# Optimization experiments

Hardware: AMD Instinct MI355X
Metric: run time of the kernel (lower is better)

The kernel has to match this reference:

```python
import jax, jax.numpy as jnp
import numpy as np

N_NODES = 100000
N_EDGES = 1600000
IN_SIZE = 128
HIDDEN = 32
OUT_SIZE = 16


def _mean_agg(h, src, dst, n_nodes):
    # segment-sum of source features into destination nodes, then divide by in-degree
    summed = jax.ops.segment_sum(h[src], dst, num_segments=n_nodes)  # [N, D]
    deg = jax.ops.segment_sum(jnp.ones((src.shape[0],), h.dtype), dst, num_segments=n_nodes)
    return summed / jnp.maximum(deg, 1.0)[:, None]


def _sage_layer(h, src, dst, W_self, W_neigh, b):
    # DGL SAGEConv (mean): fc_self(h) + fc_neigh(mean_neigh(h)) + bias
    agg = _mean_agg(h, src, dst, h.shape[0])
    return h @ W_self + agg @ W_neigh + b


def setup_inputs() -> dict:
    key = jax.random.key(0)
    ks = jax.random.split(key, 9)
    inp = {
        "x": jax.random.normal(ks[0], (N_NODES, IN_SIZE), jnp.float32),
        "edge_src": jax.random.randint(ks[1], (N_EDGES,), 0, N_NODES, jnp.int32),
        "edge_dst": jax.random.randint(ks[2], (N_EDGES,), 0, N_NODES, jnp.int32),
        "W_self1": jax.random.normal(ks[3], (IN_SIZE, HIDDEN), jnp.float32) / np.sqrt(IN_SIZE),
        "W_neigh1": jax.random.normal(ks[4], (IN_SIZE, HIDDEN), jnp.float32) / np.sqrt(IN_SIZE),
        "b1": jnp.zeros((HIDDEN,), jnp.float32),
        "W_self2": jax.random.normal(ks[5], (HIDDEN, HIDDEN), jnp.float32) / np.sqrt(HIDDEN),
        "W_neigh2": jax.random.normal(ks[6], (HIDDEN, HIDDEN), jnp.float32) / np.sqrt(HIDDEN),
        "b2": jnp.zeros((HIDDEN,), jnp.float32),
        "W_self3": jax.random.normal(ks[7], (HIDDEN, OUT_SIZE), jnp.float32) / np.sqrt(HIDDEN),
        "W_neigh3": jax.random.normal(ks[8], (HIDDEN, OUT_SIZE), jnp.float32) / np.sqrt(HIDDEN),
        "b3": jnp.zeros((OUT_SIZE,), jnp.float32),
    }
    return inp


def reference(x, edge_src, edge_dst,
              W_self1, W_neigh1, b1,
              W_self2, W_neigh2, b2,
              W_self3, W_neigh3, b3):
    h = jax.nn.relu(_sage_layer(x, edge_src, edge_dst, W_self1, W_neigh1, b1))
    h = jax.nn.relu(_sage_layer(h, edge_src, edge_dst, W_self2, W_neigh2, b2))
    h = _sage_layer(h, edge_src, edge_dst, W_self3, W_neigh3, b3)
    return h
```

## Files before the change

### kernel.cpp

```cpp
#include <hip/hip_runtime.h>


#define BLOCK 256
#define NBLK 256
#define BSH 9
#define CAP 12288

__device__ __forceinline__ unsigned pack_bf16(float a, float b) {
    unsigned ua = __float_as_uint(a); ua = (ua + 0x7fffu + ((ua >> 16) & 1u)) >> 16;
    unsigned ub = __float_as_uint(b); ub = (ub + 0x7fffu + ((ub >> 16) & 1u)) >> 16;
    return ua | (ub << 16);
}

__global__ void hist_kernel(const int* __restrict__ dst, int* __restrict__ hist,
                            int n_edges, int nbuk, int ch) {
    __shared__ int cnt[256];
    int tid = threadIdx.x;
    for (int i = tid; i < nbuk; i += BLOCK) cnt[i] = 0;
    __syncthreads();
    int e0 = blockIdx.x * ch;
    int e1 = e0 + ch; if (e1 > n_edges) e1 = n_edges;
    for (int e = e0 + tid; e < e1; e += BLOCK)
        atomicAdd(&cnt[dst[e] >> BSH], 1);
    __syncthreads();
    for (int i = tid; i < nbuk; i += BLOCK)
        hist[i * NBLK + blockIdx.x] = cnt[i];
}

__global__ void scanBlk_kernel(int* __restrict__ hist, int* __restrict__ buktot) {
    int b = blockIdx.x;
    int tid = threadIdx.x;
    int orig = hist[b * NBLK + tid];
    int v = orig;
    int lane = tid & 63, w = tid >> 6;
#pragma unroll
    for (int off = 1; off < 64; off <<= 1) {
        int u = __shfl_up(v, off);
        if (lane >= off) v += u;
    }
    __shared__ int wps[4];
    if (lane == 63) wps[w] = v;
    __syncthreads();
    int wadd = 0;
    for (int k = 0; k < w; ++k) wadd += wps[k];
    int excl = v - orig + wadd;
    hist[b * NBLK + tid] = excl;
    if (tid == 255) buktot[b] = excl + orig;
}

__global__ void scanBuk_kernel(const int* __restrict__ buktot, int* __restrict__ bukoff,
                               int nbuk, int* __restrict__ startp, int n_nodes, int n_edges) {
    int tid = threadIdx.x;
    int orig = (tid < nbuk) ? buktot[tid] : 0;
    int v = orig;
    int lane = tid & 63, w = tid >> 6;
#pragma unroll
    for (int off = 1; off < 64; off <<= 1) {
        int u = __shfl_up(v, off);
        if (lane >= off) v += u;
    }
    __shared__ int wps[4];
    if (lane == 63) wps[w] = v;
    __syncthreads();
    int wadd = 0;
    for (int k = 0; k < w; ++k) wadd += wps[k];
    int excl = v - orig + wadd;
    if (tid < nbuk) bukoff[tid] = excl;
    if (tid == 0) { bukoff[nbuk] = n_edges; startp[n_nodes] = n_edges; }
}

__global__ void part_kernel(const int* __restrict__ src, const int* __restrict__ dst,
                            const int* __restrict__ hist, const int* __restrict__ bukoff,
                            unsigned* __restrict__ pairs, int n_edges, int nbuk, int ch) {
    __shared__ int base[256];
    __shared__ int cnt[256];
    int tid = threadIdx.x;
    for (int i = tid; i < nbuk; i += BLOCK) {
        base[i] = hist[i * NBLK + blockIdx.x] + bukoff[i];
        cnt[i] = 0;
    }
    __syncthreads();
    int e0 = blockIdx.x * ch;
    int e1 = e0 + ch; if (e1 > n_edges) e1 = n_edges;
    for (int e = e0 + tid; e < e1; e += BLOCK) {
        int d = dst[e];
        int b = d >> BSH;
        unsigned dl = (unsigned)(d & ((1 << BSH) - 1));
        int r = atomicAdd(&cnt[b], 1);
        pairs[base[b] + r] = (unsigned)src[e] | (dl << 20);
    }
}

__global__ void build_kernel(const unsigned* __restrict__ pairs, const int* __restrict__ bukoff,
                             int* __restrict__ start, float* __restrict__ invdeg,
                             int* __restrict__ csr_src, int n_nodes) {
    __shared__ int deg[512];
    __shared__ int lst[512];
    __shared__ int cur[512];
    __shared__ int wps[4];
    __shared__ int scsr[CAP];

    int b = blockIdx.x;
    int tid = threadIdx.x;
    int e0 = bukoff[b];
    int e1 = bukoff[b + 1];
    int lo = b << BSH;
    int hi = lo + (1 << BSH); if (hi > n_nodes) hi = n_nodes;
    int nn = hi - lo;
    int ne = e1 - e0;

    for (int i = tid; i < 512; i += BLOCK) deg[i] = 0;
    __syncthreads();
    for (int i = e0 + tid; i < e1; i += BLOCK)
        atomicAdd(&deg[pairs[i] >> 20], 1);
    __syncthreads();

    int d0 = deg[2 * tid], d1 = deg[2 * tid + 1];
    int s = d0 + d1;
    int lane = tid & 63, w = tid >> 6;
    int v = s;
#pragma unroll
    for (int off = 1; off < 64; off <<= 1) {
        int u = __shfl_up(v, off);
        if (lane >= off) v += u;
    }
    if (lane == 63) wps[w] = v;
    __syncthreads();
    int wb = 0;
    for (int k = 0; k < w; ++k) wb += wps[k];
    int excl = wb + v - s;
    lst[2 * tid] = excl;
    lst[2 * tid + 1] = excl + d0;
    cur[2 * tid] = 0;
    cur[2 * tid + 1] = 0;
    __syncthreads();

    for (int i = tid; i < nn; i += BLOCK) {
        start[lo + i] = e0 + lst[i];
        int d = deg[i];
        invdeg[lo + i] = 1.0f / (float)(d < 1 ? 1 : d);
    }

    if (ne <= CAP) {
        for (int i = e0 + tid; i < e1; i += BLOCK) {
            unsigned pr = pairs[i];
            int dl = pr >> 20;
            int sl = lst[dl] + atomicAdd(&cur[dl], 1);
            scsr[sl] = (int)(pr & 0xFFFFFu);
        }
        __syncthreads();
        for (int i = tid; i < ne; i += BLOCK) csr_src[e0 + i] = scsr[i];
    } else {
        for (int i = e0 + tid; i < e1; i += BLOCK) {
            unsigned pr = pairs[i];
            int dl = pr >> 20;
            int sl = lst[dl] + atomicAdd(&cur[dl], 1);
            csr_src[e0 + sl] = (int)(pr & 0xFFFFFu);
        }
    }
}

template<int DIN, int DOUT, int OPT, int NPT>
__global__ __launch_bounds__(256, 4)
void proj_reg(const float* __restrict__ h,
              const float* __restrict__ Ws,
              const float* __restrict__ Wn,
              const float* __restrict__ bias,
              float* __restrict__ pre,
              unsigned short* __restrict__ p,
              int n_nodes) {
    constexpr int OD  = 2 * DOUT;
    constexpr int OG  = OD / OPT;
    constexpr int NG  = 256 / OG;
    constexpr int NT  = NPT * NG;
    constexpr int NV  = OPT / 4;

    __shared__ float sW[DIN][OD];
    __shared__ float sb[DOUT];

    const int tid = threadIdx.x;
    for (int i = tid; i < DIN * OD; i += 256) {
        int k = i / OD, o = i % OD;
        sW[k][o] = (o < DOUT) ? Ws[k * DOUT + o] : Wn[k * DOUT + (o - DOUT)];
    }
    if (tid < DOUT) sb[tid] = bias[tid];
    __syncthreads();

    const int to = tid % OG;
    const int tn = tid / OG;
    const int o0 = to * OPT;
    const int node0 = blockIdx.x * NT + tn * NPT;

    const float4* __restrict__ xp[NPT];
#pragma unroll
    for (int n = 0; n < NPT; ++n) {
        int node = node0 + n;
        int safe = (node < n_nodes) ? node : (n_nodes - 1);
        xp[n] = reinterpret_cast<const float4*>(h + (size_t)safe * DIN);
    }

    float acc[NPT][OPT];
#pragma unroll
    for (int n = 0; n < NPT; ++n)
#pragma unroll
        for (int o = 0; o < OPT; ++o) acc[n][o] = 0.f;

#pragma unroll 2
    for (int k4 = 0; k4 < DIN / 4; ++k4) {
        float4 xv[NPT];
#pragma unroll
        for (int n = 0; n < NPT; ++n) xv[n] = xp[n][k4];
#pragma unroll
        for (int kk = 0; kk < 4; kk += 2) {
            int k = 4 * k4 + kk;
            float4 w0[NV], w1[NV];
#pragma unroll
            for (int v = 0; v < NV; ++v) {
                w0[v] = *reinterpret_cast<const float4*>(&sW[k][o0 + 4 * v]);
                w1[v] = *reinterpret_cast<const float4*>(&sW[k + 1][o0 + 4 * v]);
            }
#pragma unroll
            for (int n = 0; n < NPT; ++n) {
                float xk = reinterpret_cast<const float*>(&xv[n])[kk];
#pragma unroll
                for (int v = 0; v < NV; ++v) {
                    acc[n][4 * v + 0] = fmaf(xk, w0[v].x, acc[n][4 * v + 0]);
                    acc[n][4 * v + 1] = fmaf(xk, w0[v].y, acc[n][4 * v + 1]);
                    acc[n][4 * v + 2] = fmaf(xk, w0[v].z, acc[n][4 * v + 2]);
                    acc[n][4 * v + 3] = fmaf(xk, w0[v].w, acc[n][4 * v + 3]);
                }
            }
#pragma unroll
            for (int n = 0; n < NPT; ++n) {
                float xk = reinterpret_cast<const float*>(&xv[n])[kk + 1];
#pragma unroll
                for (int v = 0; v < NV; ++v) {
                    acc[n][4 * v + 0] = fmaf(xk, w1[v].x, acc[n][4 * v + 0]);
                    acc[n][4 * v + 1] = fmaf(xk, w1[v].y, acc[n][4 * v + 1]);
                    acc[n][4 * v + 2] = fmaf(xk, w1[v].z, acc[n][4 * v + 2]);
                    acc[n][4 * v + 3] = fmaf(xk, w1[v].w, acc[n][4 * v + 3]);
                }
            }
        }
    }

    const bool self_half = (o0 < DOUT);
    const int oo = self_half ? o0 : (o0 - DOUT);
#pragma unroll
    for (int n = 0; n < NPT; ++n) {
        int node = node0 + n;
        if (node >= n_nodes) continue;
        if (self_half) {
#pragma unroll
            for (int v = 0; v < NV; ++v) {
                float4 r;
                r.x = acc[n][4 * v + 0] + sb[oo + 4 * v + 0];
                r.y = acc[n][4 * v + 1] + sb[oo + 4 * v + 1];
                r.z = acc[n][4 * v + 2] + sb[oo + 4 * v + 2];
                r.w = acc[n][4 * v + 3] + sb[oo + 4 * v + 3];
                *reinterpret_cast<float4*>(pre + (size_t)node * DOUT + oo + 4 * v) = r;
            }
        } else {
            unsigned uw[OPT / 2];
#pragma unroll
            for (int v = 0; v < OPT / 2; ++v)
                uw[v] = pack_bf16(acc[n][2 * v], acc[n][2 * v + 1]);
            unsigned short* dstp = p + (size_t)node * DOUT + oo;
            if (OPT == 8) {
                *reinterpret_cast<uint4*>(dstp) = make_uint4(uw[0], uw[1], uw[2], uw[3]);
            } else {
                *reinterpret_cast<uint2*>(dstp) = make_uint2(uw[0], uw[1]);
            }
        }
    }
}

template<int D, bool RELU>
__global__ void gather_kernel(const unsigned short* __restrict__ p,
                              const int* __restrict__ csr_src,
                              const int* __restrict__ start,
                              const float* __restrict__ pre,
                              const float* __restrict__ invdeg,
                              float* __restrict__ out,
                              int n_nodes) {
    constexpr int NPW = 64 / D;
    int wave = threadIdx.x >> 6;
    int lane = threadIdx.x & 63;
    int g = (blockIdx.x * (blockDim.x >> 6) + wave) * NPW + lane / D;
    int f = lane % D;
    if (g >= n_nodes) return;
    int s0 = start[g];
    int s1 = start[g + 1];
    float a0 = 0.f, a1 = 0.f, a2 = 0.f, a3 = 0.f;
    float a4 = 0.f, a5 = 0.f, a6 = 0.f, a7 = 0.f;
    int j = s0;
    for (; j + 8 <= s1; j += 8) {
        int c0 = csr_src[j + 0], c1 = csr_src[j + 1];
        int c2 = csr_src[j + 2], c3 = csr_src[j + 3];
        int c4 = csr_src[j + 4], c5 = csr_src[j + 5];
        int c6 = csr_src[j + 6], c7 = csr_src[j + 7];
        unsigned short u0 = p[(size_t)c0 * D + f];
        unsigned short u1 = p[(size_t)c1 * D + f];
        unsigned short u2 = p[(size_t)c2 * D + f];
        unsigned short u3 = p[(size_t)c3 * D + f];
        unsigned short u4 = p[(size_t)c4 * D + f];
        unsigned short u5 = p[(size_t)c5 * D + f];
        unsigned short u6 = p[(size_t)c6 * D + f];
        unsigned short u7 = p[(size_t)c7 * D + f];
        a0 += __uint_as_float((unsigned)u0 << 16);
        a1 += __uint_as_float((unsigned)u1 << 16);
        a2 += __uint_as_float((unsigned)u2 << 16);
        a3 += __uint_as_float((unsigned)u3 << 16);
        a4 += __uint_as_float((unsigned)u4 << 16);
        a5 += __uint_as_float((unsigned)u5 << 16);
        a6 += __uint_as_float((unsigned)u6 << 16);
        a7 += __uint_as_float((unsigned)u7 << 16);
    }
    for (; j + 2 <= s1; j += 2) {
        int c0 = csr_src[j], c1 = csr_src[j + 1];
        a0 += __uint_as_float((unsigned)p[(size_t)c0 * D + f] << 16);
        a1 += __uint_as_float((unsigned)p[(size_t)c1 * D + f] << 16);
    }
    if (j < s1)
        a2 += __uint_as_float((unsigned)p[(size_t)csr_src[j] * D + f] << 16);
    float a = ((a0 + a1) + (a2 + a3)) + ((a4 + a5) + (a6 + a7));
    size_t o = (size_t)g * D + f;
    float v = pre[o] + a * invdeg[g];
    if (RELU) v = fmaxf(v, 0.f);
    out[o] = v;
}

extern "C" void kernel_launch(void* const* d_in, const int* in_sizes, int n_in,
                              void* d_out, int out_size, void* d_ws, size_t ws_size,
                              hipStream_t stream) {
    const float* x        = (const float*)d_in[0];
    const int*   edge_src = (const int*)d_in[1];
    const int*   edge_dst = (const int*)d_in[2];
    const float* Ws1 = (const float*)d_in[3];
    const float* Wn1 = (const float*)d_in[4];
    const float* b1  = (const float*)d_in[5];
    const float* Ws2 = (const float*)d_in[6];
    const float* Wn2 = (const float*)d_in[7];
    const float* b2  = (const float*)d_in[8];
    const float* Ws3 = (const float*)d_in[9];
    const float* Wn3 = (const float*)d_in[10];
    const float* b3  = (const float*)d_in[11];
    float* out = (float*)d_out;

    const int IN = 128, HID = 32;
    const int n_nodes = in_sizes[0] / IN;
    const int n_edges = in_sizes[1];
    const int nbuk = (n_nodes + (1 << BSH) - 1) >> BSH;
    const int ch   = (n_edges + NBLK - 1) / NBLK;

    char* wsb = (char*)d_ws;
    size_t off = 0;
    auto alloc = [&](size_t bytes) { char* r = wsb + off; off = (off + bytes + 255) & ~(size_t)255; return r; };
    int*   startp = (int*)alloc(((size_t)n_nodes + 1) * sizeof(int));
    float* invdeg = (float*)alloc((size_t)n_nodes * sizeof(float));
    int*   csr    = (int*)alloc((size_t)n_edges * sizeof(int));
    int*   hist   = (int*)alloc((size_t)nbuk * NBLK * sizeof(int));
    int*   buktot = (int*)alloc(256 * sizeof(int));
    int*   bukoff = (int*)alloc(257 * sizeof(int));
    float* B0     = (float*)alloc((size_t)n_nodes * HID * sizeof(float));
    unsigned short* B1 = (unsigned short*)alloc((size_t)n_nodes * HID * 2);
    float* B3     = (float*)alloc((size_t)n_nodes * HID * sizeof(float));
    unsigned* pairs = (unsigned*)B0;

    const int gP     = (n_nodes + 63) / 64;
    const int gGat32 = (n_nodes + 7) / 8;
    const int gGat16 = (n_nodes + 15) / 16;

    hist_kernel   <<<NBLK, BLOCK, 0, stream>>>(edge_dst, hist, n_edges, nbuk, ch);
    scanBlk_kernel<<<nbuk, BLOCK, 0, stream>>>(hist, buktot);
    scanBuk_kernel<<<1, BLOCK, 0, stream>>>(buktot, bukoff, nbuk, startp, n_nodes, n_edges);
    part_kernel   <<<NBLK, BLOCK, 0, stream>>>(edge_src, edge_dst, hist, bukoff, pairs, n_edges, nbuk, ch);
    build_kernel  <<<nbuk, BLOCK, 0, stream>>>(pairs, bukoff, startp, invdeg, csr, n_nodes);

    proj_reg<128, 32, 8, 2><<<gP, BLOCK, 0, stream>>>(x, Ws1, Wn1, b1, B0, B1, n_nodes);
    gather_kernel<32, true><<<gGat32, BLOCK, 0, stream>>>(B1, csr, startp, B0, invdeg, B3, n_nodes);

    proj_reg<32, 32, 8, 2><<<gP, BLOCK, 0, stream>>>(B3, Ws2, Wn2, b2, B0, B1, n_nodes);
    gather_kernel<32, true><<<gGat32, BLOCK, 0, stream>>>(B1, csr, startp, B0, invdeg, B3, n_nodes);

    proj_reg<32, 16, 4, 2><<<gP, BLOCK, 0, stream>>>(B3, Ws3, Wn3, b3, B0, B1, n_nodes);
    gather_kernel<16, false><<<gGat16, BLOCK, 0, stream>>>(B1, csr, startp, B0, invdeg, out, n_nodes);
}
```

Baseline: 196.3 us.

## Use bf16 MFMA for node projections and store hidden activations as bf16

```diff
diff --git a/kernel.cpp b/kernel.cpp
--- a/kernel.cpp
+++ b/kernel.cpp
@@ -6,10 +6,17 @@
 #define BSH 9
 #define CAP 12288
 
+typedef __attribute__((ext_vector_type(8))) short bf16x8;
+typedef __attribute__((ext_vector_type(4))) float f32x4;
+
 __device__ __forceinline__ unsigned pack_bf16(float a, float b) {
     unsigned ua = __float_as_uint(a); ua = (ua + 0x7fffu + ((ua >> 16) & 1u)) >> 16;
     unsigned ub = __float_as_uint(b); ub = (ub + 0x7fffu + ((ub >> 16) & 1u)) >> 16;
     return ua | (ub << 16);
+}
+__device__ __forceinline__ unsigned short bf16r(float f) {
+    unsigned u = __float_as_uint(f);
+    return (unsigned short)((u + 0x7fffu + ((u >> 16) & 1u)) >> 16);
 }
 
 __global__ void hist_kernel(const int* __restrict__ dst, int* __restrict__ hist,
@@ -160,128 +167,138 @@
     }
 }
 
-template<int DIN, int DOUT, int OPT, int NPT>
+__global__ void prep_kernel(const float* __restrict__ Ws1, const float* __restrict__ Wn1,
+                            const float* __restrict__ Ws2, const float* __restrict__ Wn2,
+                            const float* __restrict__ Ws3, const float* __restrict__ Wn3,
+                            unsigned short* __restrict__ Wt1,
+                            unsigned short* __restrict__ Wt2,
+                            unsigned short* __restrict__ Wt3) {
+    int stride = gridDim.x * BLOCK;
+    int t0 = blockIdx.x * BLOCK + threadIdx.x;
+    for (int i = t0; i < 64 * 128; i += stride) {
+        int o = i / 128, k = i % 128;
+        float v = (o < 32) ? Ws1[k * 32 + o] : Wn1[k * 32 + (o - 32)];
+        Wt1[i] = bf16r(v);
+    }
+    for (int i = t0; i < 64 * 32; i += stride) {
+        int o = i / 32, k = i % 32;
+        float v = (o < 32) ? Ws2[k * 32 + o] : Wn2[k * 32 + (o - 32)];
+        Wt2[i] = bf16r(v);
+    }
+    for (int i = t0; i < 32 * 32; i += stride) {
+        int o = i / 32, k = i % 32;
+        float v = (o < 16) ? Ws3[k * 16 + o] : Wn3[k * 16 + (o - 16)];
+        Wt3[i] = bf16r(v);
+    }
+}
+
 __global__ __launch_bounds__(256, 4)
-void proj_reg(const float* __restrict__ h,
-              const float* __restrict__ Ws,
-              const float* __restrict__ Wn,
-              const float* __restrict__ bias,
-              float* __restrict__ pre,
-              unsigned short* __restrict__ p,
-              int n_nodes) {
-    constexpr int OD  = 2 * DOUT;
-    constexpr int OG  = OD / OPT;
-    constexpr int NG  = 256 / OG;
-    constexpr int NT  = NPT * NG;
-    constexpr int NV  = OPT / 4;
-
-    __shared__ float sW[DIN][OD];
-    __shared__ float sb[DOUT];
-
-    const int tid = threadIdx.x;
-    for (int i = tid; i < DIN * OD; i += 256) {
-        int k = i / OD, o = i % OD;
-        sW[k][o] = (o < DOUT) ? Ws[k * DOUT + o] : Wn[k * DOUT + (o - DOUT)];
-    }
-    if (tid < DOUT) sb[tid] = bias[tid];
-    __syncthreads();
-
-    const int to = tid % OG;
-    const int tn = tid / OG;
-    const int o0 = to * OPT;
-    const int node0 = blockIdx.x * NT + tn * NPT;
-
-    const float4* __restrict__ xp[NPT];
-#pragma unroll
-    for (int n = 0; n < NPT; ++n) {
-        int node = node0 + n;
-        int safe = (node < n_nodes) ? node : (n_nodes - 1);
-        xp[n] = reinterpret_cast<const float4*>(h + (size_t)safe * DIN);
-    }
-
-    float acc[NPT][OPT];
-#pragma unroll
-    for (int n = 0; n < NPT; ++n)
-#pragma unroll
-        for (int o = 0; o < OPT; ++o) acc[n][o] = 0.f;
-
-#pragma unroll 2
-    for (int k4 = 0; k4 < DIN / 4; ++k4) {
-        float4 xv[NPT];
-#pragma unroll
-        for (int n = 0; n < NPT; ++n) xv[n] = xp[n][k4];
-#pragma unroll
-        for (int kk = 0; kk < 4; kk += 2) {
-            int k = 4 * k4 + kk;
-            float4 w0[NV], w1[NV];
-#pragma unroll
-            for (int v = 0; v < NV; ++v) {
-                w0[v] = *reinterpret_cast<const float4*>(&sW[k][o0 + 4 * v]);
-                w1[v] = *reinterpret_cast<const float4*>(&sW[k + 1][o0 + 4 * v]);
-            }
-#pragma unroll
-            for (int n = 0; n < NPT; ++n) {
-                float xk = reinterpret_cast<const float*>(&xv[n])[kk];
-#pragma unroll
-                for (int v = 0; v < NV; ++v) {
-                    acc[n][4 * v + 0] = fmaf(xk, w0[v].x, acc[n][4 * v + 0]);
-                    acc[n][4 * v + 1] = fmaf(xk, w0[v].y, acc[n][4 * v + 1]);
-                    acc[n][4 * v + 2] = fmaf(xk, w0[v].z, acc[n][4 * v + 2]);
-                    acc[n][4 * v + 3] = fmaf(xk, w0[v].w, acc[n][4 * v + 3]);
-                }
-            }
-#pragma unroll
-            for (int n = 0; n < NPT; ++n) {
-                float xk = reinterpret_cast<const float*>(&xv[n])[kk + 1];
-#pragma unroll
-                for (int v = 0; v < NV; ++v) {
-                    acc[n][4 * v + 0] = fmaf(xk, w1[v].x, acc[n][4 * v + 0]);
-                    acc[n][4 * v + 1] = fmaf(xk, w1[v].y, acc[n][4 * v + 1]);
-                    acc[n][4 * v + 2] = fmaf(xk, w1[v].z, acc[n][4 * v + 2]);
-                    acc[n][4 * v + 3] = fmaf(xk, w1[v].w, acc[n][4 * v + 3]);
-                }
+void proj1_mfma(const float* __restrict__ x,
+                const unsigned short* __restrict__ Wt,
+                const float* __restrict__ bias,
+                float* __restrict__ pre,
+                unsigned short* __restrict__ p,
+                int n_nodes) {
+    int tid = threadIdx.x;
+    int wv = tid >> 6, l = tid & 63;
+    int col = l & 15, kg = l >> 4;
+    int node0 = blockIdx.x * 64 + wv * 16;
+
+    int arow = node0 + col;
+    if (arow >= n_nodes) arow = n_nodes - 1;
+    const float* xr = x + (size_t)arow * 128 + kg * 8;
+
+    f32x4 acc[4];
+#pragma unroll
+    for (int t = 0; t < 4; ++t) acc[t] = (f32x4){0.f, 0.f, 0.f, 0.f};
+
+#pragma unroll
+    for (int ks = 0; ks < 4; ++ks) {
+        float4 f0 = *reinterpret_cast<const float4*>(xr + ks * 32);
+        float4 f1 = *reinterpret_cast<const float4*>(xr + ks * 32 + 4);
+        union { bf16x8 v; unsigned u[4]; } A;
+        A.u[0] = pack_bf16(f0.x, f0.y);
+        A.u[1] = pack_bf16(f0.z, f0.w);
+        A.u[2] = pack_bf16(f1.x, f1.y);
+        A.u[3] = pack_bf16(f1.z, f1.w);
+#pragma unroll
+        for (int t = 0; t < 4; ++t) {
+            bf16x8 B = *reinterpret_cast<const bf16x8*>(
+                Wt + (size_t)(t * 16 + col) * 128 + ks * 32 + kg * 8);
+            acc[t] = __builtin_amdgcn_mfma_f32_16x16x32_bf16(A.v, B, acc[t], 0, 0, 0);
+        }
+    }
+
+    int nodeb = node0 + kg * 4;
+#pragma unroll
+    for (int t = 0; t < 4; ++t) {
+        int out = t * 16 + col;
+#pragma unroll
+        for (int r = 0; r < 4; ++r) {
+            int node = nodeb + r;
+            if (node >= n_nodes) continue;
+            if (t < 2) {
+                pre[(size_t)node * 32 + out] = acc[t][r] + bias[out];
+            } else {
+                p[(size_t)node * 32 + (out - 32)] = bf16r(acc[t][r]);
             }
         }
     }
-
-    const bool self_half = (o0 < DOUT);
-    const int oo = self_half ? o0 : (o0 - DOUT);
-#pragma unroll
-    for (int n = 0; n < NPT; ++n) {
-        int node = node0 + n;
-        if (node >= n_nodes) continue;
-        if (self_half) {
-#pragma unroll
-            for (int v = 0; v < NV; ++v) {
-                float4 r;
-                r.x = acc[n][4 * v + 0] + sb[oo + 4 * v + 0];
-                r.y = acc[n][4 * v + 1] + sb[oo + 4 * v + 1];
-                r.z = acc[n][4 * v + 2] + sb[oo + 4 * v + 2];
-                r.w = acc[n][4 * v + 3] + sb[oo + 4 * v + 3];
-                *reinterpret_cast<float4*>(pre + (size_t)node * DOUT + oo + 4 * v) = r;
-            }
-        } else {
-            unsigned uw[OPT / 2];
-#pragma unroll
-            for (int v = 0; v < OPT / 2; ++v)
-                uw[v] = pack_bf16(acc[n][2 * v], acc[n][2 * v + 1]);
-            unsigned short* dstp = p + (size_t)node * DOUT + oo;
-            if (OPT == 8) {
-                *reinterpret_cast<uint4*>(dstp) = make_uint4(uw[0], uw[1], uw[2], uw[3]);
+}
+
+template<int DOUT>
+__global__ __launch_bounds__(256, 4)
+void proj23_mfma(const unsigned short* __restrict__ h,
+                 const unsigned short* __restrict__ Wt,
+                 const float* __restrict__ bias,
+                 float* __restrict__ pre,
+                 unsigned short* __restrict__ p,
+                 int n_nodes) {
+    constexpr int NTILE = DOUT / 8;
+    int tid = threadIdx.x;
+    int wv = tid >> 6, l = tid & 63;
+    int col = l & 15, kg = l >> 4;
+    int node0 = blockIdx.x * 64 + wv * 16;
+
+    int arow = node0 + col;
+    if (arow >= n_nodes) arow = n_nodes - 1;
+    bf16x8 A = *reinterpret_cast<const bf16x8*>(h + (size_t)arow * 32 + kg * 8);
+
+    f32x4 acc[NTILE];
+#pragma unroll
+    for (int t = 0; t < NTILE; ++t) acc[t] = (f32x4){0.f, 0.f, 0.f, 0.f};
+
+#pragma unroll
+    for (int t = 0; t < NTILE; ++t) {
+        bf16x8 B = *reinterpret_cast<const bf16x8*>(
+            Wt + (size_t)(t * 16 + col) * 32 + kg * 8);
+        acc[t] = __builtin_amdgcn_mfma_f32_16x16x32_bf16(A, B, acc[t], 0, 0, 0);
+    }
+
+    int nodeb = node0 + kg * 4;
+#pragma unroll
+    for (int t = 0; t < NTILE; ++t) {
+        int out = t * 16 + col;
+#pragma unroll
+        for (int r = 0; r < 4; ++r) {
+            int node = nodeb + r;
+            if (node >= n_nodes) continue;
+            if (out < DOUT) {
+                pre[(size_t)node * DOUT + out] = acc[t][r] + bias[out];
             } else {
-                *reinterpret_cast<uint2*>(dstp) = make_uint2(uw[0], uw[1]);
+                p[(size_t)node * DOUT + (out - DOUT)] = bf16r(acc[t][r]);
             }
         }
     }
 }
 
-template<int D, bool RELU>
+template<int D, bool RELU, bool BF16OUT>
 __global__ void gather_kernel(const unsigned short* __restrict__ p,
                               const int* __restrict__ csr_src,
                               const int* __restrict__ start,
                               const float* __restrict__ pre,
                               const float* __restrict__ invdeg,
-                              float* __restrict__ out,
+                              void* __restrict__ outv,
                               int n_nodes) {
     constexpr int NPW = 64 / D;
     int wave = threadIdx.x >> 6;
@@ -299,22 +316,14 @@
         int c2 = csr_src[j + 2], c3 = csr_src[j + 3];
         int c4 = csr_src[j + 4], c5 = csr_src[j + 5];
         int c6 = csr_src[j + 6], c7 = csr_src[j + 7];
-        unsigned short u0 = p[(size_t)c0 * D + f];
-        unsigned short u1 = p[(size_t)c1 * D + f];
-        unsigned short u2 = p[(size_t)c2 * D + f];
-        unsigned short u3 = p[(size_t)c3 * D + f];
-        unsigned short u4 = p[(size_t)c4 * D + f];
-        unsigned short u5 = p[(size_t)c5 * D + f];
-        unsigned short u6 = p[(size_t)c6 * D + f];
-        unsigned short u7 = p[(size_t)c7 * D + f];
-        a0 += __uint_as_float((unsigned)u0 << 16);
-        a1 += __uint_as_float((unsigned)u1 << 16);
-        a2 += __uint_as_float((unsigned)u2 << 16);
-        a3 += __uint_as_float((unsigned)u3 << 16);
-        a4 += __uint_as_float((unsigned)u4 << 16);
-        a5 += __uint_as_float((unsigned)u5 << 16);
-        a6 += __uint_as_float((unsigned)u6 << 16);
-        a7 += __uint_as_float((unsigned)u7 << 16);
+        a0 += __uint_as_float((unsigned)p[(size_t)c0 * D + f] << 16);
+        a1 += __uint_as_float((unsigned)p[(size_t)c1 * D + f] << 16);
+        a2 += __uint_as_float((unsigned)p[(size_t)c2 * D + f] << 16);
+        a3 += __uint_as_float((unsigned)p[(size_t)c3 * D + f] << 16);
+        a4 += __uint_as_float((unsigned)p[(size_t)c4 * D + f] << 16);
+        a5 += __uint_as_float((unsigned)p[(size_t)c5 * D + f] << 16);
+        a6 += __uint_as_float((unsigned)p[(size_t)c6 * D + f] << 16);
+        a7 += __uint_as_float((unsigned)p[(size_t)c7 * D + f] << 16);
     }
     for (; j + 2 <= s1; j += 2) {
         int c0 = csr_src[j], c1 = csr_src[j + 1];
@@ -327,7 +336,11 @@
     size_t o = (size_t)g * D + f;
     float v = pre[o] + a * invdeg[g];
     if (RELU) v = fmaxf(v, 0.f);
-    out[o] = v;
+    if (BF16OUT) {
+        ((unsigned short*)outv)[o] = bf16r(v);
+    } else {
+        ((float*)outv)[o] = v;
+    }
 }
 
 extern "C" void kernel_launch(void* const* d_in, const int* in_sizes, int n_in,
@@ -362,27 +375,31 @@
     int*   hist   = (int*)alloc((size_t)nbuk * NBLK * sizeof(int));
     int*   buktot = (int*)alloc(256 * sizeof(int));
     int*   bukoff = (int*)alloc(257 * sizeof(int));
+    unsigned short* Wt1 = (unsigned short*)alloc(64 * 128 * 2);
+    unsigned short* Wt2 = (unsigned short*)alloc(64 * 32 * 2);
+    unsigned short* Wt3 = (unsigned short*)alloc(32 * 32 * 2);
     float* B0     = (float*)alloc((size_t)n_nodes * HID * sizeof(float));
     unsigned short* B1 = (unsigned short*)alloc((size_t)n_nodes * HID * 2);
-    float* B3     = (float*)alloc((size_t)n_nodes * HID * sizeof(float));
+    unsigned short* B3 = (unsigned short*)alloc((size_t)n_nodes * HID * 2);
     unsigned* pairs = (unsigned*)B0;
 
     const int gP     = (n_nodes + 63) / 64;
     const int gGat32 = (n_nodes + 7) / 8;
     const int gGat16 = (n_nodes + 15) / 16;
 
+    prep_kernel   <<<64, BLOCK, 0, stream>>>(Ws1, Wn1, Ws2, Wn2, Ws3, Wn3, Wt1, Wt2, Wt3);
     hist_kernel   <<<NBLK, BLOCK, 0, stream>>>(edge_dst, hist, n_edges, nbuk, ch);
     scanBlk_kernel<<<nbuk, BLOCK, 0, stream>>>(hist, buktot);
     scanBuk_kernel<<<1, BLOCK, 0, stream>>>(buktot, bukoff, nbuk, startp, n_nodes, n_edges);
     part_kernel   <<<NBLK, BLOCK, 0, stream>>>(edge_src, edge_dst, hist, bukoff, pairs, n_edges, nbuk, ch);
     build_kernel  <<<nbuk, BLOCK, 0, stream>>>(pairs, bukoff, startp, invdeg, csr, n_nodes);
 
-    proj_reg<128, 32, 8, 2><<<gP, BLOCK, 0, stream>>>(x, Ws1, Wn1, b1, B0, B1, n_nodes);
-    gather_kernel<32, true><<<gGat32, BLOCK, 0, stream>>>(B1, csr, startp, B0, invdeg, B3, n_nodes);
-
-    proj_reg<32, 32, 8, 2><<<gP, BLOCK, 0, stream>>>(B3, Ws2, Wn2, b2, B0, B1, n_nodes);
-    gather_kernel<32, true><<<gGat32, BLOCK, 0, stream>>>(B1, csr, startp, B0, invdeg, B3, n_nodes);
-
-    proj_reg<32, 16, 4, 2><<<gP, BLOCK, 0, stream>>>(B3, Ws3, Wn3, b3, B0, B1, n_nodes);
-    gather_kernel<16, false><<<gGat16, BLOCK, 0, stream>>>(B1, csr, startp, B0, invdeg, out, n_nodes);
-}
+    proj1_mfma<<<gP, BLOCK, 0, stream>>>(x, Wt1, b1, B0, B1, n_nodes);
+    gather_kernel<32, true, true><<<gGat32, BLOCK, 0, stream>>>(B1, csr, startp, B0, invdeg, B3, n_nodes);
+
+    proj23_mfma<32><<<gP, BLOCK, 0, stream>>>(B3, Wt2, b2, B0, B1, n_nodes);
+    gather_kernel<32, true, true><<<gGat32, BLOCK, 0, stream>>>(B1, csr, startp, B0, invdeg, B3, n_nodes);
+
+    proj23_mfma<16><<<gP, BLOCK, 0, stream>>>(B3, Wt3, b3, B0, B1, n_nodes);
+    gather_kernel<16, false, false><<<gGat16, BLOCK, 0, stream>>>(B1, csr, startp, B0, invdeg, out, n_nodes);
+}
```

Result: faster. 190.5 us (-3.0%).
